# Kernel optimization log

Measured on AMD Instinct MI355X. Metric: run time of the kernel, lower is better.

The kernel has to match this reference:

```python
import jax, jax.numpy as jnp
import numpy as np

RADIUS = 1.0
NSAMPLE = 8
GROUPS = 8
EPS = 1e-5


def setup_inputs() -> dict:
    key = jax.random.key(0)
    ks = jax.random.split(key, 8)
    b, n_p, dim, C = 4, 4096, 128, 64
    coords = jax.random.normal(ks[0], (b, n_p, 3), jnp.float32)
    xyz2 = jax.random.normal(ks[1], (b, n_p, 3), jnp.float32)
    fmap1 = jax.random.normal(ks[2], (b, dim, n_p), jnp.float32)
    fmap2 = jax.random.normal(ks[3], (b, dim, n_p), jnp.float32)
    conv_w = jax.random.normal(ks[4], (C, 4), jnp.float32) * 0.1
    conv_b = jnp.zeros((C,), jnp.float32)
    gn_gamma = jnp.ones((C,), jnp.float32)
    gn_beta = jnp.zeros((C,), jnp.float32)
    prelu_a = jnp.full((1,), 0.25, jnp.float32)
    out_w = jax.random.normal(ks[5], (C, C), jnp.float32) * 0.1
    out_b = jnp.zeros((C,), jnp.float32)
    return {"coords": coords, "xyz2": xyz2, "fmap1": fmap1, "fmap2": fmap2,
            "conv_w": conv_w, "conv_b": conv_b, "gn_gamma": gn_gamma,
            "gn_beta": gn_beta, "prelu_a": prelu_a, "out_w": out_w, "out_b": out_b}


def ball_query(xyz2, coords, radius, nsample):
    # first-nsample points of xyz2 within `radius` of each query in coords,
    # padded with the first valid index (0 if none) -- matches PointNet++ ball query.
    n = xyz2.shape[1]
    d2 = jnp.sum((coords[:, :, None, :] - xyz2[:, None, :, :]) ** 2, axis=-1)  # [b,m,n]
    j = jnp.arange(n, dtype=jnp.float32)
    score = jnp.where(d2 < radius * radius, -j, -float(n))  # larger score = earlier valid idx
    vals, _ = jax.lax.top_k(score, nsample)  # [b,m,nsample]
    valid = vals > -float(n)
    idx = (-vals).astype(jnp.int32)
    first = jnp.where(valid[..., :1], idx[..., :1], 0)
    return jnp.where(valid, idx, first)  # [b,m,nsample]


def reference(coords, xyz2, fmap1, fmap2, conv_w, conv_b, gn_gamma, gn_beta, prelu_a, out_w, out_b):
    b, n_p, _ = coords.shape
    dim = fmap1.shape[1]
    # corr = fmap1^T fmap2 / sqrt(dim): [b, n_p, n_p]
    corr = jnp.einsum('bdn,bdm->bnm', fmap1, fmap2) / jnp.sqrt(jnp.float32(dim))
    idx = ball_query(xyz2, coords, RADIUS, NSAMPLE)  # [b,n_p,nsample]
    # grouped_xyz: xyz2[idx] - coords -> [b, 3, n_p, nsample]
    gathered = jax.vmap(lambda pts, ind: pts[ind])(xyz2, idx)  # [b,n_p,ns,3]
    grouped_xyz = jnp.transpose(gathered - coords[:, :, None, :], (0, 3, 1, 2))
    # corr gather along source dim
    cur_corr = jnp.take_along_axis(corr, idx, axis=2)[:, None]  # [b,1,n_p,ns]
    feat = jnp.concatenate([cur_corr, grouped_xyz], axis=1)  # [b,4,n_p,ns]
    # 1x1 Conv2d
    x = jnp.einsum('oc,bcns->bons', conv_w, feat) + conv_b[None, :, None, None]
    # GroupNorm(8, 64)
    C = x.shape[1]
    xg = x.reshape(b, GROUPS, C // GROUPS, n_p, NSAMPLE)
    mu = jnp.mean(xg, axis=(2, 3, 4), keepdims=True)
    var = jnp.var(xg, axis=(2, 3, 4), keepdims=True)
    xg = (xg - mu) * jax.lax.rsqrt(var + EPS)
    x = xg.reshape(b, C, n_p, NSAMPLE) * gn_gamma[None, :, None, None] + gn_beta[None, :, None, None]
    # PReLU (single shared slope)
    x = jnp.where(x >= 0, x, prelu_a[0] * x)
    # max over neighbors
    x = jnp.max(x, axis=3)  # [b,64,n_p]
    # 1x1 Conv1d out
    return jnp.einsum('oc,bcn->bon', out_w, x) + out_b[None, :, None]
```

## Files before the change

kernel.cpp:

```cpp
#include <hip/hip_runtime.h>
#include <math.h>

#define B 4
#define NP 4096
#define DIM 128
#define CCH 64
#define NS 8

__global__ __launch_bounds__(256) void k_transpose(
    const float* __restrict__ f2, float* __restrict__ o2) {
  int tb = blockIdx.x;
  int t = threadIdx.x;
  __shared__ float tile[128][33];
  int b = tb >> 7;
  int n0 = (tb & 127) * 32;
  const float* s = f2 + (size_t)b * DIM * NP;
  float* d = o2 + (size_t)b * NP * DIM;
  int dr = t >> 3;
  int ng = t & 7;
#pragma unroll
  for (int k = 0; k < 4; ++k) {
    int dd = dr + 32 * k;
    float4 v = *(const float4*)&s[(size_t)dd * NP + n0 + ng * 4];
    tile[dd][ng * 4 + 0] = v.x;
    tile[dd][ng * 4 + 1] = v.y;
    tile[dd][ng * 4 + 2] = v.z;
    tile[dd][ng * 4 + 3] = v.w;
  }
  __syncthreads();
  int n = t >> 3;
#pragma unroll
  for (int k = 0; k < 4; ++k) {
    int d0 = (t & 7) * 4 + 32 * k;
    float4 w;
    w.x = tile[d0 + 0][n];
    w.y = tile[d0 + 1][n];
    w.z = tile[d0 + 2][n];
    w.w = tile[d0 + 3][n];
    *(float4*)&d[(size_t)(n0 + n) * DIM + d0] = w;
  }
}

__global__ __launch_bounds__(256) void k_bqcorr(
    const float* __restrict__ coords, const float* __restrict__ xyz2,
    const float* __restrict__ f1, const float* __restrict__ f2,
    const float* __restrict__ f2T, float* __restrict__ feat,
    float* __restrict__ parts, int trans) {
  int blk = blockIdx.x;
  int t = threadIdx.x;
  int bq = (blk & 7) >> 1;
  int chunk = ((blk >> 3) << 1) | (blk & 1);
  int m0 = chunk * 16;
  __shared__ float As[16 * 132];
  __shared__ int sidx[128];
  __shared__ float red[4][14];

  if (trans) {
#pragma unroll
    for (int pass = 0; pass < 2; ++pass) {
      int d = pass * 64 + (t >> 2);
      int j4 = t & 3;
      float4 v = *(const float4*)&f1[(size_t)(bq * DIM + d) * NP + m0 + j4 * 4];
      As[(j4 * 4 + 0) * 132 + d] = v.x;
      As[(j4 * 4 + 1) * 132 + d] = v.y;
      As[(j4 * 4 + 2) * 132 + d] = v.z;
      As[(j4 * 4 + 3) * 132 + d] = v.w;
    }
  }

  {
    int wv = t >> 6, lane = t & 63;
    const float* xz = xyz2 + (size_t)bq * NP * 3;
    float cx[4], cy[4], cz[4];
#pragma unroll
    for (int qi = 0; qi < 4; ++qi) {
      const float* cp = coords + ((size_t)bq * NP + m0 + wv * 4 + qi) * 3;
      cx[qi] = cp[0]; cy[qi] = cp[1]; cz[qi] = cp[2];
    }
    int cnt[4] = {0, 0, 0, 0};
    int first[4] = {0, 0, 0, 0};
    int j0 = lane * 3;
    float ax = xz[j0], ay = xz[j0 + 1], az = xz[j0 + 2];
    int j1 = (64 + lane) * 3;
    float bx = xz[j1], by = xz[j1 + 1], bz = xz[j1 + 2];
#pragma unroll 1
    for (int c = 0; c < 64; c += 2) {
      int c2 = (c + 2 < 64) ? c + 2 : 63;
      int c3 = (c + 3 < 64) ? c + 3 : 63;
      int jn2 = (c2 * 64 + lane) * 3, jn3 = (c3 * 64 + lane) * 3;
      float nax = xz[jn2], nay = xz[jn2 + 1], naz = xz[jn2 + 2];
      float nbx = xz[jn3], nby = xz[jn3 + 1], nbz = xz[jn3 + 2];
#pragma unroll
      for (int qi = 0; qi < 4; ++qi) {
        if (cnt[qi] < NS) {
          float dx = __fsub_rn(cx[qi], ax);
          float dy = __fsub_rn(cy[qi], ay);
          float dz = __fsub_rn(cz[qi], az);
          float d2 = __fadd_rn(__fadd_rn(__fmul_rn(dx, dx), __fmul_rn(dy, dy)),
                               __fmul_rn(dz, dz));
          bool hit = d2 < 1.0f;
          unsigned long long mk = __ballot(hit);
          if (mk) {
            int rank = cnt[qi] + __popcll(mk & ((1ull << lane) - 1ull));
            if (hit && rank < NS)
              sidx[(wv * 4 + qi) * NS + rank] = c * 64 + lane;
            if (cnt[qi] == 0) first[qi] = c * 64 + (__ffsll(mk) - 1);
            cnt[qi] += __popcll(mk);
          }
        }
      }
      if ((cnt[0] >= NS) & (cnt[1] >= NS) & (cnt[2] >= NS) & (cnt[3] >= NS))
        break;
#pragma unroll
      for (int qi = 0; qi < 4; ++qi) {
        if (cnt[qi] < NS) {
          float dx = __fsub_rn(cx[qi], bx);
          float dy = __fsub_rn(cy[qi], by);
          float dz = __fsub_rn(cz[qi], bz);
          float d2 = __fadd_rn(__fadd_rn(__fmul_rn(dx, dx), __fmul_rn(dy, dy)),
                               __fmul_rn(dz, dz));
          bool hit = d2 < 1.0f;
          unsigned long long mk = __ballot(hit);
          if (mk) {
            int rank = cnt[qi] + __popcll(mk & ((1ull << lane) - 1ull));
            if (hit && rank < NS)
              sidx[(wv * 4 + qi) * NS + rank] = (c + 1) * 64 + lane;
            if (cnt[qi] == 0) first[qi] = (c + 1) * 64 + (__ffsll(mk) - 1);
            cnt[qi] += __popcll(mk);
          }
        }
      }
      if ((cnt[0] >= NS) & (cnt[1] >= NS) & (cnt[2] >= NS) & (cnt[3] >= NS))
        break;
      ax = nax; ay = nay; az = naz;
      bx = nbx; by = nby; bz = nbz;
    }
#pragma unroll
    for (int qi = 0; qi < 4; ++qi) {
      if (lane < NS && lane >= cnt[qi])
        sidx[(wv * 4 + qi) * NS + lane] = first[qi];
    }
  }
  __syncthreads();

  int g = t >> 3;
  int l = t & 7;
  float pm[14];
#pragma unroll
  for (int k = 0; k < 14; ++k) pm[k] = 0.f;

  if (trans) {
    int id0 = sidx[g], id1 = sidx[32 + g];
    int id2 = sidx[64 + g], id3 = sidx[96 + g];
    const float4* br0 = (const float4*)(f2T + ((size_t)bq * NP + id0) * DIM) + l;
    const float4* br1 = (const float4*)(f2T + ((size_t)bq * NP + id1) * DIM) + l;
    const float4* br2 = (const float4*)(f2T + ((size_t)bq * NP + id2) * DIM) + l;
    const float4* br3 = (const float4*)(f2T + ((size_t)bq * NP + id3) * DIM) + l;
    float4 y00 = br0[0], y01 = br0[8], y02 = br0[16], y03 = br0[24];
    float4 y10 = br1[0], y11 = br1[8], y12 = br1[16], y13 = br1[24];
    const float* xq0 = xyz2 + ((size_t)bq * NP + id0) * 3;
    const float* xq1 = xyz2 + ((size_t)bq * NP + id1) * 3;
    float x0x = xq0[0], x0y = xq0[1], x0z = xq0[2];
    float x1x = xq1[0], x1y = xq1[1], x1z = xq1[2];
    float4 y20 = br2[0], y21 = br2[8], y22 = br2[16], y23 = br2[24];
    float4 y30 = br3[0], y31 = br3[8], y32 = br3[16], y33 = br3[24];
    const float* xq2 = xyz2 + ((size_t)bq * NP + id2) * 3;
    const float* xq3 = xyz2 + ((size_t)bq * NP + id3) * 3;
    float x2x = xq2[0], x2y = xq2[1], x2z = xq2[2];
    float x3x = xq3[0], x3y = xq3[1], x3z = xq3[2];
    size_t fbase = ((size_t)bq * NP + m0) * NS;

#define DO_R(r, ya, yb, yc, yd, nxx, nxy, nxz)                                 \
    {                                                                          \
      int pi = (r) * 32 + g;                                                   \
      int m = pi >> 3;                                                         \
      const float4* arow = (const float4*)&As[m * 132] + l;                    \
      float4 a0 = arow[0], a1 = arow[8], a2 = arow[16], a3 = arow[24];         \
      float acc = a0.x * ya.x + a0.y * ya.y + a0.z * ya.z + a0.w * ya.w +      \
                  a1.x * yb.x + a1.y * yb.y + a1.z * yb.z + a1.w * yb.w +      \
                  a2.x * yc.x + a2.y * yc.y + a2.z * yc.z + a2.w * yc.w +      \
                  a3.x * yd.x + a3.y * yd.y + a3.z * yd.z + a3.w * yd.w;       \
      acc += __shfl_xor(acc, 1);                                               \
      acc += __shfl_xor(acc, 2);                                               \
      acc += __shfl_xor(acc, 4);                                               \
      float corr = acc * 0.08838834764831843f;                                 \
      const float* cpq = coords + ((size_t)bq * NP + m0 + m) * 3;              \
      float dx = nxx - cpq[0], dy = nxy - cpq[1], dz = nxz - cpq[2];           \
      if (l == 0) {                                                            \
        float4 fv;                                                             \
        fv.x = corr; fv.y = dx; fv.z = dy; fv.w = dz;                          \
        ((float4*)feat)[fbase + pi] = fv;                                      \
      }                                                                        \
      pm[0] += corr; pm[1] += dx; pm[2] += dy; pm[3] += dz;                    \
      pm[4] += corr * corr; pm[5] += corr * dx; pm[6] += corr * dy;            \
      pm[7] += corr * dz; pm[8] += dx * dx; pm[9] += dx * dy;                  \
      pm[10] += dx * dz; pm[11] += dy * dy; pm[12] += dy * dz;                 \
      pm[13] += dz * dz;                                                       \
    }
    DO_R(0, y00, y01, y02, y03, x0x, x0y, x0z)
    DO_R(1, y10, y11, y12, y13, x1x, x1y, x1z)
    DO_R(2, y20, y21, y22, y23, x2x, x2y, x2z)
    DO_R(3, y30, y31, y32, y33, x3x, x3y, x3z)
#undef DO_R
  } else {
    int idv[4];
#pragma unroll
    for (int r = 0; r < 4; ++r) idv[r] = sidx[r * 32 + g];
#pragma unroll
    for (int r = 0; r < 4; ++r) {
      int pi = r * 32 + g;
      int m = pi >> 3, s = pi & 7;
      int id = idv[r];
      float acc = 0.f;
#pragma unroll
      for (int k = 0; k < 4; ++k) {
#pragma unroll
        for (int c = 0; c < 4; ++c) {
          int d = (l + 8 * k) * 4 + c;
          acc += f1[(size_t)(bq * DIM + d) * NP + m0 + m] *
                 f2[(size_t)(bq * DIM + d) * NP + id];
        }
      }
      acc += __shfl_xor(acc, 1);
      acc += __shfl_xor(acc, 2);
      acc += __shfl_xor(acc, 4);
      float corr = acc * 0.08838834764831843f;
      const float* cpq = coords + ((size_t)bq * NP + m0 + m) * 3;
      const float* xp = xyz2 + ((size_t)bq * NP + id) * 3;
      float dx = xp[0] - cpq[0], dy = xp[1] - cpq[1], dz = xp[2] - cpq[2];
      if (l == 0) {
        float4 fv;
        fv.x = corr; fv.y = dx; fv.z = dy; fv.w = dz;
        ((float4*)feat)[((size_t)bq * NP + m0 + m) * NS + s] = fv;
      }
      pm[0] += corr; pm[1] += dx; pm[2] += dy; pm[3] += dz;
      pm[4] += corr * corr; pm[5] += corr * dx; pm[6] += corr * dy;
      pm[7] += corr * dz; pm[8] += dx * dx; pm[9] += dx * dy;
      pm[10] += dx * dz; pm[11] += dy * dy; pm[12] += dy * dz;
      pm[13] += dz * dz;
    }
  }

#pragma unroll
  for (int k = 0; k < 14; ++k) {
    float v = pm[k];
#pragma unroll
    for (int off = 32; off; off >>= 1) v += __shfl_xor(v, off);
    pm[k] = v;
  }
  int lane = t & 63, wvv = t >> 6;
  if (lane == 0) {
#pragma unroll
    for (int k = 0; k < 14; ++k) red[wvv][k] = pm[k];
  }
  __syncthreads();
  if (t < 14) {
    float ssum = (red[0][t] + red[1][t] + red[2][t] + red[3][t]) * 0.125f;
    parts[((size_t)bq * 256 + chunk) * 14 + t] = ssum;
  }
}

__global__ __launch_bounds__(256) void kB_out(
    const float* __restrict__ feat, const float* __restrict__ parts,
    const float* __restrict__ conv_w, const float* __restrict__ conv_b,
    const float* __restrict__ gamma, const float* __restrict__ beta,
    const float* __restrict__ prelu, const float* __restrict__ out_w,
    const float* __restrict__ out_b, float* __restrict__ out) {
  int b = blockIdx.x >> 8;
  int n0 = (blockIdx.x & 255) * 16;
  __shared__ float4 fs4[16 * 8];
  __shared__ float4 vs4[16 * 16];
  __shared__ float4 ow4[64 * 16];
  __shared__ float cw[256], cb_[64], Av[64], Bv[64], ob_[64];
  __shared__ float red2[8][14];
  __shared__ float Sm[14];
  __shared__ float SxA[64], SxxA[64];
  int t = threadIdx.x;
  if (t < 128) fs4[t] = ((const float4*)(feat + ((size_t)b * NP + n0) * 32))[t];
  {
    const float4* src = (const float4*)out_w;
#pragma unroll
    for (int k = 0; k < 4; ++k) {
      int i4 = t + k * 256;
      int oo = i4 >> 4, gg = i4 & 15;
      ow4[oo * 16 + (gg ^ ((oo >> 2) & 7))] = src[i4];
    }
  }
  cw[t] = conv_w[t];
  if (t < 64) {
    cb_[t] = conv_b[t];
    ob_[t] = out_b[t];
  }
  if (t < 112) {
    int k = t % 14, jg = t / 14;
    float s = 0.f;
    const float* pp = parts + ((size_t)b * 256 + jg * 32) * 14 + k;
#pragma unroll 8
    for (int j = 0; j < 32; ++j) s += pp[j * 14];
    red2[jg][k] = s;
  }
  float alpha = prelu[0];
  __syncthreads();
  if (t < 14) {
    float s = 0.f;
#pragma unroll
    for (int jg = 0; jg < 8; ++jg) s += red2[jg][t];
    Sm[t] = s;
  }
  __syncthreads();
  if (t < 64) {
    int o = t;
    float w0 = cw[o * 4 + 0], w1 = cw[o * 4 + 1];
    float w2 = cw[o * 4 + 2], w3 = cw[o * 4 + 3];
    float bo = cb_[o];
    const float cnt = (float)(NP * NS);
    float wS1 = w0 * Sm[0] + w1 * Sm[1] + w2 * Sm[2] + w3 * Sm[3];
    float q = w0 * w0 * Sm[4] + w1 * w1 * Sm[8] + w2 * w2 * Sm[11] +
              w3 * w3 * Sm[13] +
              2.f * (w0 * w1 * Sm[5] + w0 * w2 * Sm[6] + w0 * w3 * Sm[7] +
                     w1 * w2 * Sm[9] + w1 * w3 * Sm[10] + w2 * w3 * Sm[12]);
    SxA[o] = wS1 + bo * cnt;
    SxxA[o] = q + 2.f * bo * wS1 + bo * bo * cnt;
  }
  __syncthreads();
  if (t < 64) {
    int o = t, g = o >> 3;
    const float cnt = (float)(NP * NS);
    float sm = 0.f, s2 = 0.f;
#pragma unroll
    for (int k = 0; k < 8; ++k) {
      sm += SxA[g * 8 + k];
      s2 += SxxA[g * 8 + k];
    }
    float mean = sm / (cnt * 8.f);
    float e2 = s2 / (cnt * 8.f);
    float var = e2 - mean * mean;
    float inv = rsqrtf(var + 1e-5f);
    float A = gamma[o] * inv;
    Av[o] = A;
    Bv[o] = beta[o] - mean * A;
  }
  __syncthreads();
  {
    int o = t & 63;
    int pw = t >> 6;
    float w0 = cw[o * 4 + 0], w1 = cw[o * 4 + 1];
    float w2 = cw[o * 4 + 2], w3 = cw[o * 4 + 3];
    float A = Av[o], Bc = Bv[o], bb = cb_[o];
    float* vsf = (float*)vs4;
#pragma unroll
    for (int i = 0; i < 4; ++i) {
      int p = pw * 4 + i;
      float mx = -INFINITY;
#pragma unroll
      for (int s = 0; s < NS; ++s) {
        float4 f = fs4[p * 8 + s];
        float x = fmaf(w0, f.x, fmaf(w1, f.y, fmaf(w2, f.z, fmaf(w3, f.w, bb))));
        float y = fmaf(A, x, Bc);
        y = (y >= 0.f) ? y : alpha * y;
        mx = fmaxf(mx, y);
      }
      vsf[(p * 16 + ((o >> 2) ^ ((p >> 2) & 7))) * 4 + (o & 3)] = mx;
    }
  }
  __syncthreads();
  {
    int ti = t >> 3;
    int tj = t & 7;
    float acc[2][2];
#pragma unroll
    for (int oi = 0; oi < 2; ++oi)
#pragma unroll
      for (int pj = 0; pj < 2; ++pj) acc[oi][pj] = 0.f;
#pragma unroll
    for (int g = 0; g < 16; ++g) {
      float4 vv[2], ww[2];
#pragma unroll
      for (int pj = 0; pj < 2; ++pj) {
        int p = tj * 2 + pj;
        vv[pj] = vs4[p * 16 + (g ^ ((p >> 2) & 7))];
      }
#pragma unroll
      for (int oi = 0; oi < 2; ++oi) {
        int oo = ti * 2 + oi;
        ww[oi] = ow4[oo * 16 + (g ^ ((oo >> 2) & 7))];
      }
#pragma unroll
      for (int oi = 0; oi < 2; ++oi)
#pragma unroll
        for (int pj = 0; pj < 2; ++pj) {
          acc[oi][pj] = fmaf(ww[oi].x, vv[pj].x, acc[oi][pj]);
          acc[oi][pj] = fmaf(ww[oi].y, vv[pj].y, acc[oi][pj]);
          acc[oi][pj] = fmaf(ww[oi].z, vv[pj].z, acc[oi][pj]);
          acc[oi][pj] = fmaf(ww[oi].w, vv[pj].w, acc[oi][pj]);
        }
    }
#pragma unroll
    for (int oi = 0; oi < 2; ++oi) {
      int oo = ti * 2 + oi;
      float bb = ob_[oo];
      float2 r;
      r.x = acc[oi][0] + bb;
      r.y = acc[oi][1] + bb;
      *(float2*)&out[((size_t)b * CCH + oo) * NP + n0 + tj * 2] = r;
    }
  }
}

extern "C" void kernel_launch(void* const* d_in, const int* in_sizes, int n_in,
                              void* d_out, int out_size, void* d_ws, size_t ws_size,
                              hipStream_t stream) {
  const float* coords = (const float*)d_in[0];
  const float* xyz2 = (const float*)d_in[1];
  const float* fmap1 = (const float*)d_in[2];
  const float* fmap2 = (const float*)d_in[3];
  const float* conv_w = (const float*)d_in[4];
  const float* conv_b = (const float*)d_in[5];
  const float* gamma = (const float*)d_in[6];
  const float* beta = (const float*)d_in[7];
  const float* prelu = (const float*)d_in[8];
  const float* out_w = (const float*)d_in[9];
  const float* out_b = (const float*)d_in[10];
  float* out = (float*)d_out;
  float* ws = (float*)d_ws;

  const size_t BND = (size_t)B * NP * DIM;
  const size_t FEAT = (size_t)B * NP * NS * 4;
  const size_t PARTS = (size_t)B * 256 * 14;
  size_t needT = (BND + FEAT + PARTS + 512) * sizeof(float);
  int useT = (ws_size >= needT) ? 1 : 0;

  float* f2T = ws;
  float* featp = useT ? (f2T + BND) : ws;
  float* parts = featp + FEAT;

  if (useT)
    k_transpose<<<dim3(B * (NP / 32)), dim3(256), 0, stream>>>(fmap2, f2T);
  k_bqcorr<<<dim3(1024), dim3(256), 0, stream>>>(
      coords, xyz2, fmap1, fmap2, f2T, featp, parts, useT);
  kB_out<<<dim3(B * (NP / 16)), dim3(256), 0, stream>>>(
      featp, parts, conv_w, conv_b, gamma, beta, prelu, out_w, out_b, out);
}
```

Measured before the change: 41.22 us.

## Split ball query into its own per-query kernel fused with fmap2 transpose

Moves the ball query out of the correlation kernel into a separate pass. That pass uses one block per query, and its four waves each scan a quarter of the source points in parallel; the partial hit lists are then merged in order. The same launch also carries the fmap2 transpose blocks, and the correlation kernel now reads precomputed indices from a workspace buffer. The goal is to cut the serial scan latency of the old approach, where each wave scanned sequentially for 4 queries. The cost is 16K extra blocks, each wave scanning its full quarter up to its own early exit, and an extra index round-trip through global memory. It also depends on the workspace being large enough to hold the index buffer.

```diff
diff --git a/kernel.cpp b/kernel.cpp
--- a/kernel.cpp
+++ b/kernel.cpp
@@ -7,53 +7,134 @@
 #define CCH 64
 #define NS 8
 
-__global__ __launch_bounds__(256) void k_transpose(
-    const float* __restrict__ f2, float* __restrict__ o2) {
-  int tb = blockIdx.x;
+__global__ __launch_bounds__(256) void kA_bq_transpose(
+    const float* __restrict__ coords, const float* __restrict__ xyz2,
+    int* __restrict__ idxb, const float* __restrict__ f2,
+    float* __restrict__ o2) {
+  int blk = blockIdx.x;
   int t = threadIdx.x;
   __shared__ float tile[128][33];
-  int b = tb >> 7;
-  int n0 = (tb & 127) * 32;
-  const float* s = f2 + (size_t)b * DIM * NP;
-  float* d = o2 + (size_t)b * NP * DIM;
-  int dr = t >> 3;
-  int ng = t & 7;
-#pragma unroll
-  for (int k = 0; k < 4; ++k) {
-    int dd = dr + 32 * k;
-    float4 v = *(const float4*)&s[(size_t)dd * NP + n0 + ng * 4];
-    tile[dd][ng * 4 + 0] = v.x;
-    tile[dd][ng * 4 + 1] = v.y;
-    tile[dd][ng * 4 + 2] = v.z;
-    tile[dd][ng * 4 + 3] = v.w;
-  }
-  __syncthreads();
-  int n = t >> 3;
-#pragma unroll
-  for (int k = 0; k < 4; ++k) {
-    int d0 = (t & 7) * 4 + 32 * k;
-    float4 w;
-    w.x = tile[d0 + 0][n];
-    w.y = tile[d0 + 1][n];
-    w.z = tile[d0 + 2][n];
-    w.w = tile[d0 + 3][n];
-    *(float4*)&d[(size_t)(n0 + n) * DIM + d0] = w;
+  __shared__ int sidx[4][NS];
+  __shared__ int scnt[4];
+  if (blk < B * NP) {
+    int b = blk >> 12, m = blk & (NP - 1);
+    int wv = t >> 6, lane = t & 63;
+    const float* cp = coords + ((size_t)b * NP + m) * 3;
+    float cx = cp[0], cy = cp[1], cz = cp[2];
+    const float* xz = xyz2 + (size_t)b * NP * 3;
+    int base = wv * 1024;
+    int j0 = (base + lane) * 3;
+    float ax = xz[j0], ay = xz[j0 + 1], az = xz[j0 + 2];
+    int j1 = (base + 64 + lane) * 3;
+    float bx = xz[j1], by = xz[j1 + 1], bz = xz[j1 + 2];
+    int cnt = 0;
+#pragma unroll 1
+    for (int c = 0; c < 16; c += 2) {
+      int c2 = (c + 2 < 16) ? c + 2 : 15;
+      int c3 = (c + 3 < 16) ? c + 3 : 15;
+      int jn2 = (base + c2 * 64 + lane) * 3;
+      int jn3 = (base + c3 * 64 + lane) * 3;
+      float nax = xz[jn2], nay = xz[jn2 + 1], naz = xz[jn2 + 2];
+      float nbx = xz[jn3], nby = xz[jn3 + 1], nbz = xz[jn3 + 2];
+      {
+        float dx = __fsub_rn(cx, ax);
+        float dy = __fsub_rn(cy, ay);
+        float dz = __fsub_rn(cz, az);
+        float d2 = __fadd_rn(__fadd_rn(__fmul_rn(dx, dx), __fmul_rn(dy, dy)),
+                             __fmul_rn(dz, dz));
+        bool hit = d2 < 1.0f;
+        unsigned long long mk = __ballot(hit);
+        if (mk) {
+          int rank = cnt + __popcll(mk & ((1ull << lane) - 1ull));
+          if (hit && rank < NS) sidx[wv][rank] = base + c * 64 + lane;
+          cnt += __popcll(mk);
+        }
+      }
+      if (cnt >= NS) break;
+      {
+        float dx = __fsub_rn(cx, bx);
+        float dy = __fsub_rn(cy, by);
+        float dz = __fsub_rn(cz, bz);
+        float d2 = __fadd_rn(__fadd_rn(__fmul_rn(dx, dx), __fmul_rn(dy, dy)),
+                             __fmul_rn(dz, dz));
+        bool hit = d2 < 1.0f;
+        unsigned long long mk = __ballot(hit);
+        if (mk) {
+          int rank = cnt + __popcll(mk & ((1ull << lane) - 1ull));
+          if (hit && rank < NS) sidx[wv][rank] = base + (c + 1) * 64 + lane;
+          cnt += __popcll(mk);
+        }
+      }
+      if (cnt >= NS) break;
+      ax = nax; ay = nay; az = naz;
+      bx = nbx; by = nby; bz = nbz;
+    }
+    if (lane == 0) scnt[wv] = (cnt < NS) ? cnt : NS;
+    __syncthreads();
+    if (t < NS) {
+      int c0 = scnt[0], c1 = scnt[1], c2 = scnt[2], c3 = scnt[3];
+      int total = c0 + c1 + c2 + c3;
+      int v;
+      if (t < c0) v = sidx[0][t];
+      else if (t < c0 + c1) v = sidx[1][t - c0];
+      else if (t < c0 + c1 + c2) v = sidx[2][t - c0 - c1];
+      else if (t < total) v = sidx[3][t - c0 - c1 - c2];
+      else v = (c0 > 0) ? sidx[0][0]
+             : (c1 > 0) ? sidx[1][0]
+             : (c2 > 0) ? sidx[2][0]
+             : (c3 > 0) ? sidx[3][0] : 0;
+      idxb[((size_t)b * NP + m) * NS + t] = v;
+    }
+  } else {
+    int tb = blk - B * NP;
+    int b = tb >> 7;
+    int n0 = (tb & 127) * 32;
+    const float* s = f2 + (size_t)b * DIM * NP;
+    float* d = o2 + (size_t)b * NP * DIM;
+    int dr = t >> 3;
+    int ng = t & 7;
+#pragma unroll
+    for (int k = 0; k < 4; ++k) {
+      int dd = dr + 32 * k;
+      float4 v = *(const float4*)&s[(size_t)dd * NP + n0 + ng * 4];
+      tile[dd][ng * 4 + 0] = v.x;
+      tile[dd][ng * 4 + 1] = v.y;
+      tile[dd][ng * 4 + 2] = v.z;
+      tile[dd][ng * 4 + 3] = v.w;
+    }
+    __syncthreads();
+    int n = t >> 3;
+#pragma unroll
+    for (int k = 0; k < 4; ++k) {
+      int d0 = (t & 7) * 4 + 32 * k;
+      float4 w;
+      w.x = tile[d0 + 0][n];
+      w.y = tile[d0 + 1][n];
+      w.z = tile[d0 + 2][n];
+      w.w = tile[d0 + 3][n];
+      *(float4*)&d[(size_t)(n0 + n) * DIM + d0] = w;
+    }
   }
 }
 
-__global__ __launch_bounds__(256) void k_bqcorr(
+__global__ __launch_bounds__(256) void k_corrfeat(
     const float* __restrict__ coords, const float* __restrict__ xyz2,
     const float* __restrict__ f1, const float* __restrict__ f2,
-    const float* __restrict__ f2T, float* __restrict__ feat,
-    float* __restrict__ parts, int trans) {
+    const float* __restrict__ f2T, const int* __restrict__ idxb,
+    float* __restrict__ feat, float* __restrict__ parts, int trans) {
   int blk = blockIdx.x;
   int t = threadIdx.x;
   int bq = (blk & 7) >> 1;
   int chunk = ((blk >> 3) << 1) | (blk & 1);
   int m0 = chunk * 16;
   __shared__ float As[16 * 132];
-  __shared__ int sidx[128];
   __shared__ float red[4][14];
+
+  int g = t >> 3;
+  int l = t & 7;
+  size_t ibase = ((size_t)bq * NP + m0) * NS;
+  int id0 = idxb[ibase + g], id1 = idxb[ibase + 32 + g];
+  int id2 = idxb[ibase + 64 + g], id3 = idxb[ibase + 96 + g];
 
   if (trans) {
 #pragma unroll
@@ -68,90 +149,11 @@
     }
   }
 
-  {
-    int wv = t >> 6, lane = t & 63;
-    const float* xz = xyz2 + (size_t)bq * NP * 3;
-    float cx[4], cy[4], cz[4];
-#pragma unroll
-    for (int qi = 0; qi < 4; ++qi) {
-      const float* cp = coords + ((size_t)bq * NP + m0 + wv * 4 + qi) * 3;
-      cx[qi] = cp[0]; cy[qi] = cp[1]; cz[qi] = cp[2];
-    }
-    int cnt[4] = {0, 0, 0, 0};
-    int first[4] = {0, 0, 0, 0};
-    int j0 = lane * 3;
-    float ax = xz[j0], ay = xz[j0 + 1], az = xz[j0 + 2];
-    int j1 = (64 + lane) * 3;
-    float bx = xz[j1], by = xz[j1 + 1], bz = xz[j1 + 2];
-#pragma unroll 1
-    for (int c = 0; c < 64; c += 2) {
-      int c2 = (c + 2 < 64) ? c + 2 : 63;
-      int c3 = (c + 3 < 64) ? c + 3 : 63;
-      int jn2 = (c2 * 64 + lane) * 3, jn3 = (c3 * 64 + lane) * 3;
-      float nax = xz[jn2], nay = xz[jn2 + 1], naz = xz[jn2 + 2];
-      float nbx = xz[jn3], nby = xz[jn3 + 1], nbz = xz[jn3 + 2];
-#pragma unroll
-      for (int qi = 0; qi < 4; ++qi) {
-        if (cnt[qi] < NS) {
-          float dx = __fsub_rn(cx[qi], ax);
-          float dy = __fsub_rn(cy[qi], ay);
-          float dz = __fsub_rn(cz[qi], az);
-          float d2 = __fadd_rn(__fadd_rn(__fmul_rn(dx, dx), __fmul_rn(dy, dy)),
-                               __fmul_rn(dz, dz));
-          bool hit = d2 < 1.0f;
-          unsigned long long mk = __ballot(hit);
-          if (mk) {
-            int rank = cnt[qi] + __popcll(mk & ((1ull << lane) - 1ull));
-            if (hit && rank < NS)
-              sidx[(wv * 4 + qi) * NS + rank] = c * 64 + lane;
-            if (cnt[qi] == 0) first[qi] = c * 64 + (__ffsll(mk) - 1);
-            cnt[qi] += __popcll(mk);
-          }
-        }
-      }
-      if ((cnt[0] >= NS) & (cnt[1] >= NS) & (cnt[2] >= NS) & (cnt[3] >= NS))
-        break;
-#pragma unroll
-      for (int qi = 0; qi < 4; ++qi) {
-        if (cnt[qi] < NS) {
-          float dx = __fsub_rn(cx[qi], bx);
-          float dy = __fsub_rn(cy[qi], by);
-          float dz = __fsub_rn(cz[qi], bz);
-          float d2 = __fadd_rn(__fadd_rn(__fmul_rn(dx, dx), __fmul_rn(dy, dy)),
-                               __fmul_rn(dz, dz));
-          bool hit = d2 < 1.0f;
-          unsigned long long mk = __ballot(hit);
-          if (mk) {
-            int rank = cnt[qi] + __popcll(mk & ((1ull << lane) - 1ull));
-            if (hit && rank < NS)
-              sidx[(wv * 4 + qi) * NS + rank] = (c + 1) * 64 + lane;
-            if (cnt[qi] == 0) first[qi] = (c + 1) * 64 + (__ffsll(mk) - 1);
-            cnt[qi] += __popcll(mk);
-          }
-        }
-      }
-      if ((cnt[0] >= NS) & (cnt[1] >= NS) & (cnt[2] >= NS) & (cnt[3] >= NS))
-        break;
-      ax = nax; ay = nay; az = naz;
-      bx = nbx; by = nby; bz = nbz;
-    }
-#pragma unroll
-    for (int qi = 0; qi < 4; ++qi) {
-      if (lane < NS && lane >= cnt[qi])
-        sidx[(wv * 4 + qi) * NS + lane] = first[qi];
-    }
-  }
-  __syncthreads();
-
-  int g = t >> 3;
-  int l = t & 7;
   float pm[14];
 #pragma unroll
   for (int k = 0; k < 14; ++k) pm[k] = 0.f;
 
   if (trans) {
-    int id0 = sidx[g], id1 = sidx[32 + g];
-    int id2 = sidx[64 + g], id3 = sidx[96 + g];
     const float4* br0 = (const float4*)(f2T + ((size_t)bq * NP + id0) * DIM) + l;
     const float4* br1 = (const float4*)(f2T + ((size_t)bq * NP + id1) * DIM) + l;
     const float4* br2 = (const float4*)(f2T + ((size_t)bq * NP + id2) * DIM) + l;
@@ -169,6 +171,7 @@
     float x2x = xq2[0], x2y = xq2[1], x2z = xq2[2];
     float x3x = xq3[0], x3y = xq3[1], x3z = xq3[2];
     size_t fbase = ((size_t)bq * NP + m0) * NS;
+    __syncthreads();
 
 #define DO_R(r, ya, yb, yc, yd, nxx, nxy, nxz)                                 \
     {                                                                          \
@@ -203,9 +206,8 @@
     DO_R(3, y30, y31, y32, y33, x3x, x3y, x3z)
 #undef DO_R
   } else {
-    int idv[4];
-#pragma unroll
-    for (int r = 0; r < 4; ++r) idv[r] = sidx[r * 32 + g];
+    __syncthreads();
+    int idv[4] = {id0, id1, id2, id3};
 #pragma unroll
     for (int r = 0; r < 4; ++r) {
       int pi = r * 32 + g;
@@ -427,17 +429,20 @@
   const size_t BND = (size_t)B * NP * DIM;
   const size_t FEAT = (size_t)B * NP * NS * 4;
   const size_t PARTS = (size_t)B * 256 * 14;
-  size_t needT = (BND + FEAT + PARTS + 512) * sizeof(float);
+  size_t needT = (BND + FEAT + PARTS + 512) * sizeof(float) +
+                 (size_t)B * NP * NS * sizeof(int);
   int useT = (ws_size >= needT) ? 1 : 0;
 
   float* f2T = ws;
   float* featp = useT ? (f2T + BND) : ws;
   float* parts = featp + FEAT;
-
-  if (useT)
-    k_transpose<<<dim3(B * (NP / 32)), dim3(256), 0, stream>>>(fmap2, f2T);
-  k_bqcorr<<<dim3(1024), dim3(256), 0, stream>>>(
-      coords, xyz2, fmap1, fmap2, f2T, featp, parts, useT);
+  int* idxp = (int*)(parts + PARTS + 512);
+
+  int nblk = B * NP + (useT ? (B * (NP / 32)) : 0);
+  kA_bq_transpose<<<dim3(nblk), dim3(256), 0, stream>>>(coords, xyz2, idxp,
+                                                        fmap2, f2T);
+  k_corrfeat<<<dim3(1024), dim3(256), 0, stream>>>(
+      coords, xyz2, fmap1, fmap2, f2T, idxp, featp, parts, useT);
   kB_out<<<dim3(B * (NP / 16)), dim3(256), 0, stream>>>(
       featp, parts, conv_w, conv_b, gamma, beta, prelu, out_w, out_b, out);
 }
```

Result: slower. 42.70 us (+3.6%).
